# Kernel tuning notes

Measured on AMD Instinct MI355X. Metric: run time of the kernel, lower is better.

## Reference

```python
import jax, jax.numpy as jnp
import numpy as np

T, I, H, O = 8192, 512, 1024, 2


def setup_inputs() -> dict:
    key = jax.random.key(0)
    ks = jax.random.split(key, 7)
    s_ih = 1.0 / np.sqrt(H)
    return {
        "input_seq": jax.random.normal(ks[0], (T, I), dtype=jnp.float32),
        "W_ih": jax.random.normal(ks[1], (4 * H, I), dtype=jnp.float32) * s_ih,
        "W_hh": jax.random.normal(ks[2], (4 * H, H), dtype=jnp.float32) * s_ih,
        "b_ih": jax.random.normal(ks[3], (4 * H,), dtype=jnp.float32) * s_ih,
        "b_hh": jax.random.normal(ks[4], (4 * H,), dtype=jnp.float32) * s_ih,
        "W_lin": jax.random.normal(ks[5], (O, H), dtype=jnp.float32) * s_ih,
        "b_lin": jax.random.normal(ks[6], (O,), dtype=jnp.float32) * s_ih,
    }


def reference(input_seq, W_ih, W_hh, b_ih, b_hh, W_lin, b_lin):
    h0 = jnp.zeros((H,), dtype=input_seq.dtype)
    c0 = jnp.zeros((H,), dtype=input_seq.dtype)
    # Precompute input projections for all timesteps: (T, 4H)
    x_gates = input_seq @ W_ih.T + b_ih + b_hh

    def step(carry, xg):
        h, c = carry
        gates = xg + h @ W_hh.T  # (4H,) in PyTorch order i, f, g, o
        i_g, f_g, g_g, o_g = jnp.split(gates, 4)
        i_g = jax.nn.sigmoid(i_g)
        f_g = jax.nn.sigmoid(f_g)
        g_g = jnp.tanh(g_g)
        o_g = jax.nn.sigmoid(o_g)
        c_new = f_g * c + i_g * g_g
        h_new = o_g * jnp.tanh(c_new)
        return (h_new, c_new), h_new

    _, hs = jax.lax.scan(step, (h0, c0), x_gates)  # hs: (T, H)
    logits = hs @ W_lin.T + b_lin  # (T, O)
    return jax.nn.softmax(logits, axis=-1)
```

## Files before the change

kernel.cpp:

```cpp
#include <hip/hip_runtime.h>
#include <stdint.h>

#define T_STEPS 8192
#define IN_DIM  512
#define HID     1024
#define G4      4096
#define NBLK    64
#define NW      16

typedef unsigned long long u64;

__global__ __launch_bounds__(256) void gemm_xgates(
    const float* __restrict__ A,
    const float* __restrict__ W,
    const float* __restrict__ bih,
    const float* __restrict__ bhh,
    float* __restrict__ xg)
{
    __shared__ float At[8][128];
    __shared__ float Bt[8][128];
    const int tid = threadIdx.x;
    const int r0 = blockIdx.x * 128;
    const int t0 = blockIdx.y * 128;
    const int tx = tid & 15, ty = tid >> 4;
    const int lrow = tid >> 1;
    const int kq   = (tid & 1) * 4;

    float acc[8][8];
#pragma unroll
    for (int i = 0; i < 8; ++i)
#pragma unroll
        for (int j = 0; j < 8; ++j) acc[i][j] = 0.f;

    for (int k0 = 0; k0 < IN_DIM; k0 += 8) {
        float4 av = *(const float4*)&A[(size_t)(t0 + lrow) * IN_DIM + k0 + kq];
        float4 bv = *(const float4*)&W[(size_t)(r0 + lrow) * IN_DIM + k0 + kq];
        __syncthreads();
        At[kq + 0][lrow] = av.x; At[kq + 1][lrow] = av.y;
        At[kq + 2][lrow] = av.z; At[kq + 3][lrow] = av.w;
        Bt[kq + 0][lrow] = bv.x; Bt[kq + 1][lrow] = bv.y;
        Bt[kq + 2][lrow] = bv.z; Bt[kq + 3][lrow] = bv.w;
        __syncthreads();
#pragma unroll
        for (int k = 0; k < 8; ++k) {
            float4 a0 = *(const float4*)&At[k][ty * 8];
            float4 a1 = *(const float4*)&At[k][ty * 8 + 4];
            float4 b0 = *(const float4*)&Bt[k][tx * 8];
            float4 b1 = *(const float4*)&Bt[k][tx * 8 + 4];
            float aa[8] = {a0.x, a0.y, a0.z, a0.w, a1.x, a1.y, a1.z, a1.w};
            float bb[8] = {b0.x, b0.y, b0.z, b0.w, b1.x, b1.y, b1.z, b1.w};
#pragma unroll
            for (int i = 0; i < 8; ++i)
#pragma unroll
                for (int j = 0; j < 8; ++j) acc[i][j] += aa[i] * bb[j];
        }
    }

    float bias[8];
#pragma unroll
    for (int j = 0; j < 8; ++j) {
        int r = r0 + tx * 8 + j;
        bias[j] = bih[r] + bhh[r];
    }
#pragma unroll
    for (int i = 0; i < 8; ++i) {
        int t = t0 + ty * 8 + i;
        float4 o0 = make_float4(acc[i][0] + bias[0], acc[i][1] + bias[1],
                                acc[i][2] + bias[2], acc[i][3] + bias[3]);
        float4 o1 = make_float4(acc[i][4] + bias[4], acc[i][5] + bias[5],
                                acc[i][6] + bias[6], acc[i][7] + bias[7]);
        *(float4*)&xg[(size_t)t * G4 + r0 + tx * 8]     = o0;
        *(float4*)&xg[(size_t)t * G4 + r0 + tx * 8 + 4] = o1;
    }
}

__device__ __forceinline__ float sigm_f(float x) {
    return __builtin_amdgcn_rcpf(1.f + __expf(-x));
}
__device__ __forceinline__ float tanh_f(float x) {
    x = fminf(fmaxf(x, -15.f), 15.f);
    float e = __expf(2.f * x);
    return (e - 1.f) * __builtin_amdgcn_rcpf(e + 1.f);
}

template <int PAT>
__device__ __forceinline__ float quad_bcast(float x) {
    int v = __builtin_amdgcn_update_dpp(0, __float_as_int(x), PAT, 0xf, 0xf, true);
    return __int_as_float(v);
}

__global__ __launch_bounds__(1024, 1) void lstm_rec(
    const float* __restrict__ Whh,
    const float* __restrict__ xg,
    float* __restrict__ hs,
    u64* __restrict__ hdata)
{
    __shared__ float    chunk[NW][64];
    __shared__ float    part[2][NW][64];
    __shared__ uint32_t pflag[2][NW];

    const int tid  = threadIdx.x;
    const int b    = blockIdx.x;
    const int w    = tid >> 6;
    const int l    = tid & 63;
    const int gate = l & 3;
    const int h16  = l >> 2;
    const int grow = gate * HID + b * NW + h16;

    float4 wv[16];
    {
        const float* row = &Whh[(size_t)grow * HID + 64 * w];
#pragma unroll
        for (int k4 = 0; k4 < 16; ++k4) wv[k4] = *(const float4*)&row[4 * k4];
    }
#pragma unroll
    for (int k4 = 0; k4 < 16; ++k4)
        asm volatile("" : "+v"(wv[k4].x), "+v"(wv[k4].y),
                         "+v"(wv[k4].z), "+v"(wv[k4].w));

    if (tid < 2 * NW) ((uint32_t*)pflag)[tid] = 0;
    __syncthreads();

    const bool is_red = (w == 0);
    float c  = 0.f;
    float xv = 0.f, xn = 0.f;
    if (is_red) xv = xg[grow];

    for (int t = 0; t < T_STEPS; ++t) {
        float a0 = 0.f, a1 = 0.f, a2 = 0.f, a3 = 0.f;
        if (t > 0) {
            const u64* ptr = hdata + (((size_t)(t - 1) & 1) << 10) + 64 * w + l;
            const uint32_t want32 = (uint32_t)t;
            u64 va = __hip_atomic_load(ptr, __ATOMIC_RELAXED, __HIP_MEMORY_SCOPE_AGENT);
            u64 vb = __hip_atomic_load(ptr, __ATOMIC_RELAXED, __HIP_MEMORY_SCOPE_AGENT);
            u64 v;
            for (;;) {
                if (__all((uint32_t)(va >> 32) == want32)) { v = va; break; }
                va = __hip_atomic_load(ptr, __ATOMIC_RELAXED, __HIP_MEMORY_SCOPE_AGENT);
                if (__all((uint32_t)(vb >> 32) == want32)) { v = vb; break; }
                vb = __hip_atomic_load(ptr, __ATOMIC_RELAXED, __HIP_MEMORY_SCOPE_AGENT);
            }
            chunk[w][l] = __uint_as_float((uint32_t)v);
#pragma unroll
            for (int k4 = 0; k4 < 16; ++k4) {
                float4 h4 = *(const float4*)&chunk[w][4 * k4];
                a0 = fmaf(wv[k4].x, h4.x, a0);
                a1 = fmaf(wv[k4].y, h4.y, a1);
                a2 = fmaf(wv[k4].z, h4.z, a2);
                a3 = fmaf(wv[k4].w, h4.w, a3);
            }
        }
        const int p = t & 1;
        part[p][w][l] = (a0 + a1) + (a2 + a3);
        if (l == 0)
            __hip_atomic_store(&pflag[p][w], (uint32_t)(t + 1),
                               __ATOMIC_RELEASE, __HIP_MEMORY_SCOPE_WORKGROUP);

        if (is_red) {
            if (t + 1 < T_STEPS)
                xn = xg[(size_t)(t + 1) * G4 + grow];
            const uint32_t fw = (uint32_t)(t + 1);
            for (;;) {
                uint32_t f = (l < NW)
                    ? __hip_atomic_load(&pflag[p][l], __ATOMIC_ACQUIRE,
                                        __HIP_MEMORY_SCOPE_WORKGROUP)
                    : fw;
                if (__all(f == fw)) break;
            }
            float s0 = 0.f, s1 = 0.f, s2 = 0.f, s3 = 0.f;
#pragma unroll
            for (int ww = 0; ww < NW; ww += 4) {
                s0 += part[p][ww + 0][l];
                s1 += part[p][ww + 1][l];
                s2 += part[p][ww + 2][l];
                s3 += part[p][ww + 3][l];
            }
            float pre = ((s0 + s1) + (s2 + s3)) + xv;
            float pi = quad_bcast<0x00>(pre);
            float pf = quad_bcast<0x55>(pre);
            float pg = quad_bcast<0xAA>(pre);
            float po = quad_bcast<0xFF>(pre);
            float ig = sigm_f(pi), fg = sigm_f(pf);
            float gv = tanh_f(pg), og = sigm_f(po);
            c = fg * c + ig * gv;
            float h = og * tanh_f(c);
            if (gate == 0) {
                u64 pub = ((u64)fw << 32) | (u64)__float_as_uint(h);
                __hip_atomic_store(&hdata[((size_t)p << 10) + b * NW + h16], pub,
                                   __ATOMIC_RELAXED, __HIP_MEMORY_SCOPE_AGENT);
                hs[(size_t)(t + 1) * HID + b * NW + h16] = h;
            }
            xv = xn;
        }
    }
}

__global__ __launch_bounds__(256) void proj_softmax(
    const float* __restrict__ hs,
    const float* __restrict__ Wl,
    const float* __restrict__ bl,
    float* __restrict__ out)
{
    const int tid = threadIdx.x;
    const int w = tid >> 6, l = tid & 63;
    const int row = blockIdx.x * 4 + w;
    const float* h = &hs[(size_t)(row + 1) * HID];

    float a0 = 0.f, a1 = 0.f;
#pragma unroll
    for (int i = 0; i < 4; ++i) {
        float4 hv = *(const float4*)&h[256 * i + 4 * l];
        float4 w0 = *(const float4*)&Wl[256 * i + 4 * l];
        float4 w1 = *(const float4*)&Wl[HID + 256 * i + 4 * l];
        a0 = fmaf(hv.x, w0.x, a0); a0 = fmaf(hv.y, w0.y, a0);
        a0 = fmaf(hv.z, w0.z, a0); a0 = fmaf(hv.w, w0.w, a0);
        a1 = fmaf(hv.x, w1.x, a1); a1 = fmaf(hv.y, w1.y, a1);
        a1 = fmaf(hv.z, w1.z, a1); a1 = fmaf(hv.w, w1.w, a1);
    }
#pragma unroll
    for (int off = 1; off < 64; off <<= 1) {
        a0 += __shfl_xor(a0, off, 64);
        a1 += __shfl_xor(a1, off, 64);
    }
    if (l == 0) {
        float l0 = a0 + bl[0];
        float l1 = a1 + bl[1];
        float m  = fmaxf(l0, l1);
        float e0 = __expf(l0 - m), e1 = __expf(l1 - m);
        float inv = 1.f / (e0 + e1);
        float2 o = make_float2(e0 * inv, e1 * inv);
        *(float2*)&out[(size_t)row * 2] = o;
    }
}

extern "C" void kernel_launch(void* const* d_in, const int* in_sizes, int n_in,
                              void* d_out, int out_size, void* d_ws, size_t ws_size,
                              hipStream_t stream)
{
    const float* input = (const float*)d_in[0];
    const float* W_ih  = (const float*)d_in[1];
    const float* W_hh  = (const float*)d_in[2];
    const float* b_ih  = (const float*)d_in[3];
    const float* b_hh  = (const float*)d_in[4];
    const float* W_lin = (const float*)d_in[5];
    const float* b_lin = (const float*)d_in[6];
    float* out = (float*)d_out;

    char* ws = (char*)d_ws;
    float* hs     = (float*)ws;
    size_t hs_b   = (size_t)(T_STEPS + 1) * HID * sizeof(float);
    u64*   hdata  = (u64*)(ws + hs_b);
    size_t hd_b   = 2 * 1024 * sizeof(u64);
    float* xg     = (float*)(ws + hs_b + hd_b);


    dim3 g1(G4 / 128, T_STEPS / 128);
    gemm_xgates<<<g1, 256, 0, stream>>>(input, W_ih, b_ih, b_hh, xg);

    lstm_rec<<<NBLK, NW * 64, 0, stream>>>(W_hh, xg, hs, hdata);

    proj_softmax<<<T_STEPS / 4, 256, 0, stream>>>(hs, W_lin, b_lin, out);
}
```

Before: 16.46 ms.

## Let the last-arriving wave reduce partials via LDS atomic counter instead of fixed reducer

Replaces the fixed reducer wave spinning on per-wave LDS flags with an LDS fetch-add counter. Whichever wave arrives last performs the reduction, the gate nonlinearities and the h publish. The cell state moves to shared memory so any wave can update it, and every wave now prefetches its xg value. A third in-flight poll load is added to the global h spin loop. This removes the dedicated wave's spin latency on the recurrence critical path, at the cost of LDS atomics, a cell-state round trip through LDS, and relying on counter-reset ordering across the double-buffered slots.

```diff
diff --git a/kernel.cpp b/kernel.cpp
--- a/kernel.cpp
+++ b/kernel.cpp
@@ -97,7 +97,8 @@
 {
     __shared__ float    chunk[NW][64];
     __shared__ float    part[2][NW][64];
-    __shared__ uint32_t pflag[2][NW];
+    __shared__ uint32_t cnt[2];
+    __shared__ float    cbuf[NW];
 
     const int tid  = threadIdx.x;
     const int b    = blockIdx.x;
@@ -118,27 +119,33 @@
         asm volatile("" : "+v"(wv[k4].x), "+v"(wv[k4].y),
                          "+v"(wv[k4].z), "+v"(wv[k4].w));
 
-    if (tid < 2 * NW) ((uint32_t*)pflag)[tid] = 0;
+    if (tid < 2) cnt[tid] = 0;
+    if (tid < NW) cbuf[tid] = 0.f;
     __syncthreads();
 
-    const bool is_red = (w == 0);
-    float c  = 0.f;
-    float xv = 0.f, xn = 0.f;
-    if (is_red) xv = xg[grow];
+    float xv = xg[grow];
 
     for (int t = 0; t < T_STEPS; ++t) {
+        const int p = t & 1;
+
+        float xn = 0.f;
+        if (t + 1 < T_STEPS) xn = xg[(size_t)(t + 1) * G4 + grow];
+
         float a0 = 0.f, a1 = 0.f, a2 = 0.f, a3 = 0.f;
         if (t > 0) {
             const u64* ptr = hdata + (((size_t)(t - 1) & 1) << 10) + 64 * w + l;
             const uint32_t want32 = (uint32_t)t;
             u64 va = __hip_atomic_load(ptr, __ATOMIC_RELAXED, __HIP_MEMORY_SCOPE_AGENT);
             u64 vb = __hip_atomic_load(ptr, __ATOMIC_RELAXED, __HIP_MEMORY_SCOPE_AGENT);
+            u64 vc = __hip_atomic_load(ptr, __ATOMIC_RELAXED, __HIP_MEMORY_SCOPE_AGENT);
             u64 v;
             for (;;) {
                 if (__all((uint32_t)(va >> 32) == want32)) { v = va; break; }
                 va = __hip_atomic_load(ptr, __ATOMIC_RELAXED, __HIP_MEMORY_SCOPE_AGENT);
                 if (__all((uint32_t)(vb >> 32) == want32)) { v = vb; break; }
                 vb = __hip_atomic_load(ptr, __ATOMIC_RELAXED, __HIP_MEMORY_SCOPE_AGENT);
+                if (__all((uint32_t)(vc >> 32) == want32)) { v = vc; break; }
+                vc = __hip_atomic_load(ptr, __ATOMIC_RELAXED, __HIP_MEMORY_SCOPE_AGENT);
             }
             chunk[w][l] = __uint_as_float((uint32_t)v);
 #pragma unroll
@@ -150,23 +157,16 @@
                 a3 = fmaf(wv[k4].w, h4.w, a3);
             }
         }
-        const int p = t & 1;
         part[p][w][l] = (a0 + a1) + (a2 + a3);
+
+        uint32_t tk = 0;
         if (l == 0)
-            __hip_atomic_store(&pflag[p][w], (uint32_t)(t + 1),
-                               __ATOMIC_RELEASE, __HIP_MEMORY_SCOPE_WORKGROUP);
-
-        if (is_red) {
-            if (t + 1 < T_STEPS)
-                xn = xg[(size_t)(t + 1) * G4 + grow];
-            const uint32_t fw = (uint32_t)(t + 1);
-            for (;;) {
-                uint32_t f = (l < NW)
-                    ? __hip_atomic_load(&pflag[p][l], __ATOMIC_ACQUIRE,
-                                        __HIP_MEMORY_SCOPE_WORKGROUP)
-                    : fw;
-                if (__all(f == fw)) break;
-            }
+            tk = __hip_atomic_fetch_add(&cnt[p], 1u, __ATOMIC_ACQ_REL,
+                                        __HIP_MEMORY_SCOPE_WORKGROUP);
+        tk = (uint32_t)__builtin_amdgcn_readfirstlane((int)tk);
+
+        if (tk == NW - 1) {
+            float cprev = cbuf[h16];
             float s0 = 0.f, s1 = 0.f, s2 = 0.f, s3 = 0.f;
 #pragma unroll
             for (int ww = 0; ww < NW; ww += 4) {
@@ -182,16 +182,19 @@
             float po = quad_bcast<0xFF>(pre);
             float ig = sigm_f(pi), fg = sigm_f(pf);
             float gv = tanh_f(pg), og = sigm_f(po);
-            c = fg * c + ig * gv;
-            float h = og * tanh_f(c);
+            float cn = fg * cprev + ig * gv;
+            float hn = og * tanh_f(cn);
+            const uint32_t tag = (uint32_t)(t + 1);
             if (gate == 0) {
-                u64 pub = ((u64)fw << 32) | (u64)__float_as_uint(h);
+                cbuf[h16] = cn;
+                u64 pub = ((u64)tag << 32) | (u64)__float_as_uint(hn);
                 __hip_atomic_store(&hdata[((size_t)p << 10) + b * NW + h16], pub,
                                    __ATOMIC_RELAXED, __HIP_MEMORY_SCOPE_AGENT);
-                hs[(size_t)(t + 1) * HID + b * NW + h16] = h;
-            }
-            xv = xn;
+                hs[(size_t)(t + 1) * HID + b * NW + h16] = hn;
+            }
+            if (l == 0) cnt[p] = 0;
         }
+        xv = xn;
     }
 }
 
```

Result: slower. 18.67 ms (+13.5%).

## Replace per-wave partial buffers with LDS atomic accumulation and a counter

Applied to the files above, without the earlier changes.

Within each block, each of the 16 waves now adds its partial dot product into a shared LDS accumulator with atomicAdd and bumps a shared counter. The reducer wave spins on that single counter instead of polling 16 per-wave flags and summing 16 partials. The reducer wave also gets raised scheduling priority, and the global poll loop keeps a third load in flight. The float atomics make the summation order nondeterministic, and resetting the accumulator and counter inside the reducer wave opens a possible race with the parity-buffered next use.

```diff
diff --git a/kernel.cpp b/kernel.cpp
--- a/kernel.cpp
+++ b/kernel.cpp
@@ -96,8 +96,8 @@
     u64* __restrict__ hdata)
 {
     __shared__ float    chunk[NW][64];
-    __shared__ float    part[2][NW][64];
-    __shared__ uint32_t pflag[2][NW];
+    __shared__ float    acc[2][64];
+    __shared__ uint32_t cnt[2];
 
     const int tid  = threadIdx.x;
     const int b    = blockIdx.x;
@@ -118,27 +118,34 @@
         asm volatile("" : "+v"(wv[k4].x), "+v"(wv[k4].y),
                          "+v"(wv[k4].z), "+v"(wv[k4].w));
 
-    if (tid < 2 * NW) ((uint32_t*)pflag)[tid] = 0;
+    if (tid < 2 * 64) ((float*)acc)[tid] = 0.f;
+    if (tid < 2) cnt[tid] = 0;
     __syncthreads();
 
     const bool is_red = (w == 0);
+    if (is_red) __builtin_amdgcn_s_setprio(1);
     float c  = 0.f;
     float xv = 0.f, xn = 0.f;
     if (is_red) xv = xg[grow];
 
     for (int t = 0; t < T_STEPS; ++t) {
+        const int p = t & 1;
+
         float a0 = 0.f, a1 = 0.f, a2 = 0.f, a3 = 0.f;
         if (t > 0) {
             const u64* ptr = hdata + (((size_t)(t - 1) & 1) << 10) + 64 * w + l;
             const uint32_t want32 = (uint32_t)t;
             u64 va = __hip_atomic_load(ptr, __ATOMIC_RELAXED, __HIP_MEMORY_SCOPE_AGENT);
             u64 vb = __hip_atomic_load(ptr, __ATOMIC_RELAXED, __HIP_MEMORY_SCOPE_AGENT);
+            u64 vc = __hip_atomic_load(ptr, __ATOMIC_RELAXED, __HIP_MEMORY_SCOPE_AGENT);
             u64 v;
             for (;;) {
                 if (__all((uint32_t)(va >> 32) == want32)) { v = va; break; }
                 va = __hip_atomic_load(ptr, __ATOMIC_RELAXED, __HIP_MEMORY_SCOPE_AGENT);
                 if (__all((uint32_t)(vb >> 32) == want32)) { v = vb; break; }
                 vb = __hip_atomic_load(ptr, __ATOMIC_RELAXED, __HIP_MEMORY_SCOPE_AGENT);
+                if (__all((uint32_t)(vc >> 32) == want32)) { v = vc; break; }
+                vc = __hip_atomic_load(ptr, __ATOMIC_RELAXED, __HIP_MEMORY_SCOPE_AGENT);
             }
             chunk[w][l] = __uint_as_float((uint32_t)v);
 #pragma unroll
@@ -150,32 +157,19 @@
                 a3 = fmaf(wv[k4].w, h4.w, a3);
             }
         }
-        const int p = t & 1;
-        part[p][w][l] = (a0 + a1) + (a2 + a3);
+        atomicAdd(&acc[p][l], (a0 + a1) + (a2 + a3));
         if (l == 0)
-            __hip_atomic_store(&pflag[p][w], (uint32_t)(t + 1),
-                               __ATOMIC_RELEASE, __HIP_MEMORY_SCOPE_WORKGROUP);
+            __hip_atomic_fetch_add(&cnt[p], 1u, __ATOMIC_RELEASE,
+                                   __HIP_MEMORY_SCOPE_WORKGROUP);
 
         if (is_red) {
             if (t + 1 < T_STEPS)
                 xn = xg[(size_t)(t + 1) * G4 + grow];
-            const uint32_t fw = (uint32_t)(t + 1);
-            for (;;) {
-                uint32_t f = (l < NW)
-                    ? __hip_atomic_load(&pflag[p][l], __ATOMIC_ACQUIRE,
-                                        __HIP_MEMORY_SCOPE_WORKGROUP)
-                    : fw;
-                if (__all(f == fw)) break;
-            }
-            float s0 = 0.f, s1 = 0.f, s2 = 0.f, s3 = 0.f;
-#pragma unroll
-            for (int ww = 0; ww < NW; ww += 4) {
-                s0 += part[p][ww + 0][l];
-                s1 += part[p][ww + 1][l];
-                s2 += part[p][ww + 2][l];
-                s3 += part[p][ww + 3][l];
-            }
-            float pre = ((s0 + s1) + (s2 + s3)) + xv;
+            while (__hip_atomic_load(&cnt[p], __ATOMIC_ACQUIRE,
+                                     __HIP_MEMORY_SCOPE_WORKGROUP) != NW) { }
+            float pre = acc[p][l] + xv;
+            acc[p][l] = 0.f;
+            if (l == 0) cnt[p] = 0;
             float pi = quad_bcast<0x00>(pre);
             float pf = quad_bcast<0x55>(pre);
             float pg = quad_bcast<0xAA>(pre);
@@ -184,8 +178,9 @@
             float gv = tanh_f(pg), og = sigm_f(po);
             c = fg * c + ig * gv;
             float h = og * tanh_f(c);
+            const uint32_t tag = (uint32_t)(t + 1);
             if (gate == 0) {
-                u64 pub = ((u64)fw << 32) | (u64)__float_as_uint(h);
+                u64 pub = ((u64)tag << 32) | (u64)__float_as_uint(h);
                 __hip_atomic_store(&hdata[((size_t)p << 10) + b * NW + h16], pub,
                                    __ATOMIC_RELAXED, __HIP_MEMORY_SCOPE_AGENT);
                 hs[(size_t)(t + 1) * HID + b * NW + h16] = h;
```

New measurement: 26.51 ms. +61.1%, slower.
